# Optimization experiments

Measured on AMD Instinct MI355X. Metric: run time of the kernel, lower is better.

The kernel has to match this reference:

```python
import jax, jax.numpy as jnp
import numpy as np

B, S, T = 4, 512, 512
D, F, L, H, V = 512, 2048, 6, 8, 32000
HD = D // H


def setup_inputs() -> dict:
    key = jax.random.key(0)
    ks = list(jax.random.split(key, 16))
    it = iter(ks)

    def w(shape, scale=0.02):
        return jax.random.normal(next(it), shape, jnp.float32) * scale

    enc_in = jax.random.randint(next(it), (B, S), 0, V, dtype=jnp.int32)
    dec_in = jax.random.randint(next(it), (B, T), 0, V, dtype=jnp.int32)

    # sinusoidal positional encoding (make_sine_pos_encoding)
    pos = np.arange(S)[:, None].astype(np.float32)
    i = np.arange(D)[None, :].astype(np.float32)
    angle = pos / np.power(10000.0, (2.0 * np.floor(i / 2.0)) / D)
    pe = np.zeros((S, D), np.float32)
    pe[:, 0::2] = np.sin(angle[:, 0::2])
    pe[:, 1::2] = np.cos(angle[:, 1::2])

    return {
        "enc_in": enc_in,
        "dec_in": dec_in,
        "e_embed": w((V, D)),
        "d_embed": w((V, D)),
        "pos_enc": jnp.asarray(pe),
        "enc_mha_W": w((L, 4, D, D)),      # q,k,v,out
        "enc_mha_b": jnp.zeros((L, 4, D), jnp.float32),
        "enc_ln_g": jnp.ones((L, 2, D), jnp.float32),
        "enc_ln_b": jnp.zeros((L, 2, D), jnp.float32),
        "enc_ffn_W1": w((L, D, F)),
        "enc_ffn_b1": jnp.zeros((L, F), jnp.float32),
        "enc_ffn_W2": w((L, F, D)),
        "enc_ffn_b2": jnp.zeros((L, D), jnp.float32),
        "dec_mha_W": w((L, 8, D, D)),      # self q,k,v,out then cross q,k,v,out
        "dec_mha_b": jnp.zeros((L, 8, D), jnp.float32),
        "dec_ln_g": jnp.ones((L, 3, D), jnp.float32),
        "dec_ln_b": jnp.zeros((L, 3, D), jnp.float32),
        "dec_ffn_W1": w((L, D, F)),
        "dec_ffn_b1": jnp.zeros((L, F), jnp.float32),
        "dec_ffn_W2": w((L, F, D)),
        "dec_ffn_b2": jnp.zeros((L, D), jnp.float32),
    }


def _layer_norm(x, g, b, eps=1e-6):
    m = jnp.mean(x, axis=-1, keepdims=True)
    v = jnp.mean(jnp.square(x - m), axis=-1, keepdims=True)
    return (x - m) * jax.lax.rsqrt(v + eps) * g + b


def _split_heads(x):
    b, n, _ = x.shape
    return x.reshape(b, n, H, HD).transpose(0, 2, 1, 3)  # b h n d


def _mha(xq, xkv, W, b, mask):
    # W: [>=4, D, D] slice of (q,k,v,out); mask: broadcastable to [b,h,nq,nk]
    q = _split_heads(xq @ W[0] + b[0])
    k = _split_heads(xkv @ W[1] + b[1])
    v = _split_heads(xkv @ W[2] + b[2])
    s = jnp.einsum('bhqd,bhkd->bhqk', q, k) / jnp.sqrt(jnp.float32(HD))
    s = s + mask * (-1e9)
    a = jax.nn.softmax(s, axis=-1)
    o = jnp.einsum('bhqk,bhkd->bhqd', a, v)
    o = o.transpose(0, 2, 1, 3).reshape(xq.shape[0], xq.shape[1], D)
    return o @ W[3] + b[3]


def _forward(enc_in, dec_in, e_embed, d_embed, pos_enc,
             enc_mha_W, enc_mha_b, enc_ln_g, enc_ln_b,
             enc_ffn_W1, enc_ffn_b1, enc_ffn_W2, enc_ffn_b2,
             dec_mha_W, dec_mha_b, dec_ln_g, dec_ln_b,
             dec_ffn_W1, dec_ffn_b1, dec_ffn_W2, dec_ffn_b2):
    # masks: 1.0 where attention is blocked
    enc_pad = (enc_in == 0).astype(jnp.float32)[:, None, None, :]   # [B,1,1,S]
    dec_pad = (dec_in == 0).astype(jnp.float32)[:, None, None, :]   # [B,1,1,T]
    la = jnp.triu(jnp.ones((T, T), jnp.float32), k=1)[None, None]   # [1,1,T,T]
    look_ahead = jnp.maximum(la, dec_pad)                           # [B,1,T,T]

    scale = jnp.float32(D) ** 0.5
    e = e_embed[enc_in] * scale + pos_enc[None, :S]
    d = d_embed[dec_in] * scale + pos_enc[None, :T]

    for l in range(L):
        y = _mha(e, e, enc_mha_W[l], enc_mha_b[l], enc_pad)
        e = _layer_norm(e + y, enc_ln_g[l, 0], enc_ln_b[l, 0])
        y = jax.nn.relu(e @ enc_ffn_W1[l] + enc_ffn_b1[l]) @ enc_ffn_W2[l] + enc_ffn_b2[l]
        e = _layer_norm(e + y, enc_ln_g[l, 1], enc_ln_b[l, 1])

    for l in range(L):
        y = _mha(d, d, dec_mha_W[l, 0:4], dec_mha_b[l, 0:4], look_ahead)
        d = _layer_norm(d + y, dec_ln_g[l, 0], dec_ln_b[l, 0])
        y = _mha(d, e, dec_mha_W[l, 4:8], dec_mha_b[l, 4:8], enc_pad)
        d = _layer_norm(d + y, dec_ln_g[l, 1], dec_ln_b[l, 1])
        y = jax.nn.relu(d @ dec_ffn_W1[l] + dec_ffn_b1[l]) @ dec_ffn_W2[l] + dec_ffn_b2[l]
        d = _layer_norm(d + y, dec_ln_g[l, 2], dec_ln_b[l, 2])

    return d @ d_embed.T  # [B,T,V] logits


def reference(enc_in, dec_in, e_embed, d_embed, pos_enc,
              enc_mha_W, enc_mha_b, enc_ln_g, enc_ln_b,
              enc_ffn_W1, enc_ffn_b1, enc_ffn_W2, enc_ffn_b2,
              dec_mha_W, dec_mha_b, dec_ln_g, dec_ln_b,
              dec_ffn_W1, dec_ffn_b1, dec_ffn_W2, dec_ffn_b2):
    return _forward(enc_in, dec_in, e_embed, d_embed, pos_enc,
                    enc_mha_W, enc_mha_b, enc_ln_g, enc_ln_b,
                    enc_ffn_W1, enc_ffn_b1, enc_ffn_W2, enc_ffn_b2,
                    dec_mha_W, dec_mha_b, dec_ln_g, dec_ln_b,
                    dec_ffn_W1, dec_ffn_b1, dec_ffn_W2, dec_ffn_b2)
```

## Files before the change

### kernel.cpp

```cpp
#include <hip/hip_runtime.h>
#include <hip/hip_bf16.h>
#include <math.h>

#define B_ 4
#define S_ 512
#define D_ 512
#define F_ 2048
#define L_ 6
#define H_ 8
#define V_ 32000

typedef unsigned short u16;
typedef __attribute__((ext_vector_type(8))) short bhalf8;
typedef __attribute__((ext_vector_type(4))) float f32x4;

__device__ __forceinline__ u16 f2b(float v) {
    unsigned x = __builtin_bit_cast(unsigned, v);
    return (u16)((x + 0x7FFFu + ((x >> 16) & 1u)) >> 16);
}

#define GLD16(g, l) __builtin_amdgcn_global_load_lds( \
    (const __attribute__((address_space(1))) void*)(g), \
    (__attribute__((address_space(3))) void*)(l), 16, 0, 0)

__device__ __forceinline__ float redmax16(float v) {
    #pragma unroll
    for (int m = 1; m < 16; m <<= 1) v = fmaxf(v, __shfl_xor(v, m));
    return v;
}
__device__ __forceinline__ float redsum16(float v) {
    #pragma unroll
    for (int m = 1; m < 16; m <<= 1) v += __shfl_xor(v, m);
    return v;
}

template<int NWR, int NWC, int WM, int WN, int OUT, int RELU, int MLOOP, int SPLITA>
__global__ __launch_bounds__(NWR * NWC * 64)
void mfma_gemm(const u16* __restrict__ A, const u16* __restrict__ A2, int acut,
               const u16* __restrict__ B,
               const float* __restrict__ bias, void* __restrict__ Cv,
               int K, int lda, int ldb, int ldc,
               u16* __restrict__ vtp, int vc0)
{
    constexpr int BM = NWR * WM, BN = NWC * WN;
    constexpr int NW = NWR * NWC;
    constexpr int CH_A = BM / 16, CH_B = BN / 16, CH = CH_A + CH_B;
    constexpr int NI = WM / 16, NJ = WN / 16;

    __shared__ u16 As[BM * 32];
    __shared__ u16 Bs[BN * 32];

    const int tid = threadIdx.x;
    const int wid = tid >> 6, lane = tid & 63;
    const int wrow = wid / NWC, wcol = wid % NWC;
    const long bn = (long)blockIdx.x * BN;
    const int r4 = lane >> 2, c4 = lane & 3;
    const int l15 = lane & 15, l4 = lane >> 4;

    const u16* Ause = (SPLITA && bn >= acut) ? A2 : A;

    #pragma unroll 1
    for (int mi = 0; mi < MLOOP; ++mi) {
        const long bm = ((long)blockIdx.y * MLOOP + mi) * BM;

        f32x4 acc[NI][NJ];
        #pragma unroll
        for (int i = 0; i < NI; ++i)
            #pragma unroll
            for (int j = 0; j < NJ; ++j)
                acc[i][j] = (f32x4){0.f, 0.f, 0.f, 0.f};

        for (int k0 = 0; k0 < K; k0 += 32) {
            #pragma unroll
            for (int t = 0; t < CH / NW; ++t) {
                int c = wid + t * NW;
                if (c < CH_A) {
                    const u16* g = Ause + (bm + c * 16 + r4) * (long)lda + k0 + c4 * 8;
                    GLD16(g, As + c * 512 + lane * 8);
                } else {
                    int cb = c - CH_A;
                    const u16* g = B + (bn + cb * 16 + r4) * (long)ldb + k0 + c4 * 8;
                    GLD16(g, Bs + cb * 512 + lane * 8);
                }
            }
            __syncthreads();
            bhalf8 af[NI], bfr[NJ];
            #pragma unroll
            for (int i = 0; i < NI; ++i)
                af[i] = *(const bhalf8*)&As[(wrow * WM + i * 16 + l15) * 32 + l4 * 8];
            #pragma unroll
            for (int j = 0; j < NJ; ++j)
                bfr[j] = *(const bhalf8*)&Bs[(wcol * WN + j * 16 + l15) * 32 + l4 * 8];
            #pragma unroll
            for (int i = 0; i < NI; ++i)
                #pragma unroll
                for (int j = 0; j < NJ; ++j)
                    acc[i][j] = __builtin_amdgcn_mfma_f32_16x16x32_bf16(af[i], bfr[j], acc[i][j], 0, 0, 0);
            __syncthreads();
        }

        float* Cf = (float*)Cv;
        u16*   Cb = (u16*)Cv;
        const int rowb = wrow * WM + (l4 << 2);
        const int colb = wcol * WN + l15;
        #pragma unroll
        for (int j = 0; j < NJ; ++j) {
            const long gcb = bn + wcol * WN + j * 16;
            const bool tovt = (vtp != nullptr) && (gcb >= vc0);
            const long gc = bn + colb + j * 16;
            const float bv = bias ? bias[gc] : 0.f;
            #pragma unroll
            for (int i = 0; i < NI; ++i) {
                const long gr = bm + rowb + i * 16;
                #pragma unroll
                for (int r = 0; r < 4; ++r) {
                    float v = acc[i][j][r] + bv;
                    if (RELU) v = fmaxf(v, 0.f);
                    if (tovt)          vtp[(gc - vc0) * 2048 + gr + r] = f2b(v);
                    else if (OUT == 0) Cf[(gr + r) * (long)ldc + gc] = v;
                    else               Cb[(gr + r) * (long)ldc + gc] = f2b(v);
                }
            }
        }
    }
}

template<int CAUSAL>
__global__ __launch_bounds__(256)
void flash_kernel(const u16* __restrict__ Qp, int ldq,
                  const u16* __restrict__ Kp, int ldk,
                  const u16* __restrict__ Vt,
                  const int* __restrict__ tok,
                  u16* __restrict__ Op)
{
    __shared__ u16 QS[64 * 64];
    __shared__ u16 KS[64 * 64];
    __shared__ u16 VS[64 * 64];
    __shared__ u16 PS[4 * 16 * 64];
    __shared__ float MK[512];

    const int tid = threadIdx.x, lane = tid & 63, w = tid >> 6;
    const int l15 = lane & 15, l4 = lane >> 4;
    const int qb = blockIdx.x, bh = blockIdx.y;
    const int b = bh >> 3, h = bh & 7;

    const u16* Q = Qp + (long)(b * 512 + qb * 64) * ldq + h * 64;
    const u16* K = Kp + (long)(b * 512) * ldk + h * 64;
    const u16* V = Vt + (long)(h * 64) * 2048 + b * 512;
    u16* O = Op + (long)(b * 512 + qb * 64) * 512 + h * 64;

    {
        int t0 = tok[b * 512 + tid];
        int t1 = tok[b * 512 + 256 + tid];
        MK[tid]       = (t0 == 0) ? -1e9f : 0.f;
        MK[tid + 256] = (t1 == 0) ? -1e9f : 0.f;
    }
    {
        int r = tid >> 3;
        int c = (tid & 7) ^ (r & 7);
        GLD16(Q + (long)r * ldq + c * 8,        QS + tid * 8);
        GLD16(Q + (long)(r + 32) * ldq + c * 8, QS + 2048 + tid * 8);
    }

    f32x4 oacc[4];
    float mrun[4], lrun[4];
    #pragma unroll
    for (int j = 0; j < 4; ++j) oacc[j] = (f32x4){0.f, 0.f, 0.f, 0.f};
    #pragma unroll
    for (int r = 0; r < 4; ++r) { mrun[r] = -1e30f; lrun[r] = 0.f; }

    bhalf8 qa[2];
    const int tmax = CAUSAL ? qb : 7;

    for (int t = 0; t <= tmax; ++t) {
        {
            int r = tid >> 3;
            int c = (tid & 7) ^ (r & 7);
            GLD16(K + (long)(t * 64 + r) * ldk + c * 8,       KS + tid * 8);
            GLD16(K + (long)(t * 64 + 32 + r) * ldk + c * 8,  KS + 2048 + tid * 8);
            GLD16(V + (long)r * 2048 + t * 64 + c * 8,        VS + tid * 8);
            GLD16(V + (long)(r + 32) * 2048 + t * 64 + c * 8, VS + 2048 + tid * 8);
        }
        __syncthreads();
        if (t == 0) {
            #pragma unroll
            for (int kc = 0; kc < 2; ++kc) {
                int row = w * 16 + l15;
                qa[kc] = *(const bhalf8*)&QS[row * 64 + (((kc * 4 + l4) ^ (row & 7)) << 3)];
            }
        }
        f32x4 sac[4];
        #pragma unroll
        for (int jj = 0; jj < 4; ++jj) sac[jj] = (f32x4){0.f, 0.f, 0.f, 0.f};
        bhalf8 kf[4][2];
        #pragma unroll
        for (int jj = 0; jj < 4; ++jj)
            #pragma unroll
            for (int kc = 0; kc < 2; ++kc) {
                int row = jj * 16 + l15;
                kf[jj][kc] = *(const bhalf8*)&KS[row * 64 + (((kc * 4 + l4) ^ (row & 7)) << 3)];
            }
        #pragma unroll
        for (int jj = 0; jj < 4; ++jj)
            #pragma unroll
            for (int kc = 0; kc < 2; ++kc)
                sac[jj] = __builtin_amdgcn_mfma_f32_16x16x32_bf16(qa[kc], kf[jj][kc], sac[jj], 0, 0, 0);

        #pragma unroll
        for (int jj = 0; jj < 4; ++jj) {
            float mk = MK[t * 64 + jj * 16 + l15];
            #pragma unroll
            for (int r = 0; r < 4; ++r) {
                float mk2 = mk;
                if (CAUSAL && t == qb) {
                    int col = t * 64 + jj * 16 + l15;
                    int qr = qb * 64 + w * 16 + l4 * 4 + r;
                    if (col > qr) mk2 = -1e9f;
                }
                sac[jj][r] = sac[jj][r] * 0.125f + mk2;
            }
        }
        #pragma unroll
        for (int r = 0; r < 4; ++r) {
            float mx = fmaxf(fmaxf(sac[0][r], sac[1][r]), fmaxf(sac[2][r], sac[3][r]));
            mx = redmax16(mx);
            float mnew = fmaxf(mrun[r], mx);
            float alpha = __expf(mrun[r] - mnew);
            float sum = 0.f;
            int row_p = l4 * 4 + r;
            #pragma unroll
            for (int jj = 0; jj < 4; ++jj) {
                float pv = __expf(sac[jj][r] - mnew);
                sum += pv;
                int kv = jj * 16 + l15;
                PS[w * 1024 + row_p * 64 + ((((kv >> 3) ^ (row_p & 7)) << 3) | (kv & 7))] = f2b(pv);
            }
            sum = redsum16(sum);
            lrun[r] = lrun[r] * alpha + sum;
            mrun[r] = mnew;
            #pragma unroll
            for (int jd = 0; jd < 4; ++jd) oacc[jd][r] *= alpha;
        }
        bhalf8 pa[2], vf[4][2];
        #pragma unroll
        for (int kc = 0; kc < 2; ++kc) {
            int row = l15;
            pa[kc] = *(const bhalf8*)&PS[w * 1024 + row * 64 + (((kc * 4 + l4) ^ (row & 7)) << 3)];
        }
        #pragma unroll
        for (int jd = 0; jd < 4; ++jd)
            #pragma unroll
            for (int kc = 0; kc < 2; ++kc) {
                int row = jd * 16 + l15;
                vf[jd][kc] = *(const bhalf8*)&VS[row * 64 + (((kc * 4 + l4) ^ (row & 7)) << 3)];
            }
        #pragma unroll
        for (int jd = 0; jd < 4; ++jd)
            #pragma unroll
            for (int kc = 0; kc < 2; ++kc)
                oacc[jd] = __builtin_amdgcn_mfma_f32_16x16x32_bf16(pa[kc], vf[jd][kc], oacc[jd], 0, 0, 0);
        __syncthreads();
    }

    #pragma unroll
    for (int r = 0; r < 4; ++r) {
        float inv = 1.f / lrun[r];
        int row = w * 16 + l4 * 4 + r;
        #pragma unroll
        for (int jd = 0; jd < 4; ++jd)
            O[(long)row * 512 + jd * 16 + l15] = f2b(oacc[jd][r] * inv);
    }
}

__global__ __launch_bounds__(256)
void transpose_many(const float* __restrict__ inA, const float* __restrict__ inB,
                    int zsplit, int R, int C, u16* __restrict__ out)
{
    int z = blockIdx.z;
    const float* in = (z < zsplit) ? inA + (long)z * R * C
                                   : inB + (long)(z - zsplit) * R * C;
    u16* o = out + (long)z * R * C;
    __shared__ float tb[64][65];
    const int tr = blockIdx.y * 64, tc = blockIdx.x * 64;
    const int col = threadIdx.x & 63, r0 = threadIdx.x >> 6;
    #pragma unroll
    for (int p = 0; p < 16; ++p) {
        int row = r0 * 16 + p;
        tb[row][col] = in[(long)(tr + row) * C + tc + col];
    }
    __syncthreads();
    #pragma unroll
    for (int p = 0; p < 16; ++p) {
        int row = r0 * 16 + p;
        o[(long)(tc + row) * R + tr + col] = f2b(tb[col][row]);
    }
}

__global__ __launch_bounds__(256)
void convert_b16(const float4* __restrict__ in, u16* __restrict__ out, long n4)
{
    long i = (long)blockIdx.x * 256 + threadIdx.x;
    if (i >= n4) return;
    float4 v = in[i];
    uint2 p;
    p.x = (unsigned)f2b(v.x) | ((unsigned)f2b(v.y) << 16);
    p.y = (unsigned)f2b(v.z) | ((unsigned)f2b(v.w) << 16);
    *(uint2*)(out + i * 4) = p;
}

__global__ __launch_bounds__(256)
void embed_kernel(const int* __restrict__ tE, const int* __restrict__ tD,
                  const float* __restrict__ eE, const float* __restrict__ eD,
                  const float* __restrict__ pos,
                  float* __restrict__ xE, float* __restrict__ xD,
                  u16* __restrict__ bE, u16* __restrict__ bD, float scale)
{
    const int z = blockIdx.y;
    const int* tok = z ? tD : tE;
    const float* emb = z ? eD : eE;
    float* x = z ? xD : xE;
    u16* xb = z ? bD : bE;
    int row = blockIdx.x;
    int s = row & (S_ - 1);
    int t = tok[row];
    const float* er = emb + (long)t * D_;
    const float* pr = pos + (long)s * D_;
    float* o = x + (long)row * D_;
    u16*  ob = xb + (long)row * D_;
    int i = threadIdx.x;
    float v0 = er[i]       * scale + pr[i];
    float v1 = er[i + 256] * scale + pr[i + 256];
    o[i] = v0;        o[i + 256] = v1;
    ob[i] = f2b(v0);  ob[i + 256] = f2b(v1);
}

__global__ __launch_bounds__(256)
void add_ln_kernel(float* __restrict__ x, const float* __restrict__ y,
                   u16* __restrict__ xb,
                   const float* __restrict__ g, const float* __restrict__ bb)
{
    long row = blockIdx.x;
    float* xr = x + row * D_;
    u16* xo = xb + row * D_;
    const float* yr = y + row * D_;
    int t = threadIdx.x, t2 = t + 256;

    float r0 = xr[t] + yr[t];
    float r1 = xr[t2] + yr[t2];
    float s = r0 + r1;
    float s2 = r0 * r0 + r1 * r1;
    #pragma unroll
    for (int i = 1; i < 64; i <<= 1) {
        s  += __shfl_xor(s, i);
        s2 += __shfl_xor(s2, i);
    }
    __shared__ float rs[4], rs2[4];
    int wid = t >> 6;
    if ((t & 63) == 0) { rs[wid] = s; rs2[wid] = s2; }
    __syncthreads();
    s  = rs[0] + rs[1] + rs[2] + rs[3];
    s2 = rs2[0] + rs2[1] + rs2[2] + rs2[3];

    float mean = s * (1.f / D_);
    float var  = s2 * (1.f / D_) - mean * mean;
    float inv  = rsqrtf(var + 1e-6f);
    float o0 = (r0 - mean) * inv * g[t]  + bb[t];
    float o1 = (r1 - mean) * inv * g[t2] + bb[t2];
    xr[t] = o0;       xr[t2] = o1;
    xo[t] = f2b(o0);  xo[t2] = f2b(o1);
}

extern "C" void kernel_launch(void* const* d_in, const int* in_sizes, int n_in,
                              void* d_out, int out_size, void* d_ws, size_t ws_size,
                              hipStream_t stream)
{
    const int*   enc_in     = (const int*)  d_in[0];
    const int*   dec_in     = (const int*)  d_in[1];
    const float* e_embed    = (const float*)d_in[2];
    const float* d_embed    = (const float*)d_in[3];
    const float* pos_enc    = (const float*)d_in[4];
    const float* enc_mha_W  = (const float*)d_in[5];
    const float* enc_mha_b  = (const float*)d_in[6];
    const float* enc_ln_g   = (const float*)d_in[7];
    const float* enc_ln_b   = (const float*)d_in[8];
    const float* enc_ffn_W1 = (const float*)d_in[9];
    const float* enc_ffn_b1 = (const float*)d_in[10];
    const float* enc_ffn_W2 = (const float*)d_in[11];
    const float* enc_ffn_b2 = (const float*)d_in[12];
    const float* dec_mha_W  = (const float*)d_in[13];
    const float* dec_mha_b  = (const float*)d_in[14];
    const float* dec_ln_g   = (const float*)d_in[15];
    const float* dec_ln_b   = (const float*)d_in[16];
    const float* dec_ffn_W1 = (const float*)d_in[17];
    const float* dec_ffn_b1 = (const float*)d_in[18];
    const float* dec_ffn_W2 = (const float*)d_in[19];
    const float* dec_ffn_b2 = (const float*)d_in[20];
    float* out = (float*)d_out;

    const int  BS  = B_ * S_;
    const long BSD = (long)BS * D_;
    const long DD  = (long)D_ * D_;
    const long DF  = (long)D_ * F_;

    char* p = (char*)d_ws;
    auto alloc = [&](long bytes) { char* r = p; p += (bytes + 255) & ~255L; return r; };
    float* e    = (float*)alloc(BSD * 4);
    float* dd   = (float*)alloc(BSD * 4);
    float* y    = (float*)alloc(BSD * 4);
    u16*   eb   = (u16*)  alloc(BSD * 2);
    u16*   ddb  = (u16*)  alloc(BSD * 2);
    u16*   qkv  = (u16*)  alloc((long)BS * 1536 * 2);
    u16*   att  = (u16*)  alloc(BSD * 2);
    u16*   vt   = (u16*)  alloc(BSD * 2);
    u16*   ffnh = (u16*)  alloc((long)BS * F_ * 2);
    u16*   wEmb = (u16*)  alloc((long)V_ * D_ * 2);
    u16*   wMha = (u16*)  alloc(72 * DD * 2);
    u16*   wF1  = (u16*)  alloc(12 * DF * 2);
    u16*   wF2  = (u16*)  alloc(12 * DF * 2);

    transpose_many<<<dim3(8, 8, 72), 256, 0, stream>>>(enc_mha_W, dec_mha_W, 24, 512, 512, wMha);
    transpose_many<<<dim3(32, 8, 12), 256, 0, stream>>>(enc_ffn_W1, dec_ffn_W1, 6, 512, 2048, wF1);
    transpose_many<<<dim3(8, 32, 12), 256, 0, stream>>>(enc_ffn_W2, dec_ffn_W2, 6, 2048, 512, wF2);
    convert_b16<<<16000, 256, 0, stream>>>((const float4*)d_embed, wEmb, (long)V_ * D_ / 4);

    const float scale = sqrtf((float)D_);
    embed_kernel<<<dim3(BS, 2), 256, 0, stream>>>(enc_in, dec_in, e_embed, d_embed,
                                                  pos_enc, e, dd, eb, ddb, scale);

    #define GEMM_BIG(grid, RELU, OUTT, A, Bp, bias, C, K, lda, ldb, ldc) \
        mfma_gemm<2,2,64,64,OUTT,RELU,1,0><<<grid, 256, 0, stream>>>(A, A, 1 << 30, Bp, bias, C, K, lda, ldb, ldc, nullptr, 0)
    #define GEMM_SK(grid, OUTT, A, Bp, bias, C, K, lda, ldb, ldc, vtp, vc0) \
        mfma_gemm<2,1,32,64,OUTT,0,1,0><<<grid, 128, 0, stream>>>(A, A, 1 << 30, Bp, bias, C, K, lda, ldb, ldc, vtp, vc0)

    for (int l = 0; l < L_; ++l) {
        const u16* Wl = wMha + (long)l * 4 * DD;
        const float* bl = enc_mha_b + (long)l * 4 * D_;
        GEMM_SK(dim3(24, 32), 1, eb, Wl, bl, qkv, 512, 512, 512, 1536, vt, 1024);
        flash_kernel<0><<<dim3(8, 32), 256, 0, stream>>>(qkv, 1536, qkv + 512, 1536, vt, enc_in, att);
        GEMM_SK(dim3(8, 32), 0, att, Wl + 3 * DD, bl + 3 * D_, y, 512, 512, 512, 512, nullptr, 0);
        add_ln_kernel<<<BS, 256, 0, stream>>>(e, y, eb,
            enc_ln_g + (long)(l * 2) * D_, enc_ln_b + (long)(l * 2) * D_);
        GEMM_BIG(dim3(16, 16), 1, 1, eb, wF1 + (long)l * DF, enc_ffn_b1 + (long)l * F_,
                 ffnh, 512, 512, 512, 2048);
        GEMM_SK(dim3(8, 32), 0, ffnh, wF2 + (long)l * DF, enc_ffn_b2 + (long)l * D_,
                y, 2048, 2048, 2048, 512, nullptr, 0);
        add_ln_kernel<<<BS, 256, 0, stream>>>(e, y, eb,
            enc_ln_g + (long)(l * 2 + 1) * D_, enc_ln_b + (long)(l * 2 + 1) * D_);
    }

    for (int l = 0; l < L_; ++l) {
        const u16* Wl = wMha + (long)(24 + l * 8) * DD;
        const float* bl = dec_mha_b + (long)l * 8 * D_;
        GEMM_SK(dim3(24, 32), 1, ddb, Wl, bl, qkv, 512, 512, 512, 1536, vt, 1024);
        flash_kernel<1><<<dim3(8, 32), 256, 0, stream>>>(qkv, 1536, qkv + 512, 1536, vt, dec_in, att);
        GEMM_SK(dim3(8, 32), 0, att, Wl + 3 * DD, bl + 3 * D_, y, 512, 512, 512, 512, nullptr, 0);
        add_ln_kernel<<<BS, 256, 0, stream>>>(dd, y, ddb,
            dec_ln_g + (long)(l * 3) * D_, dec_ln_b + (long)(l * 3) * D_);
        mfma_gemm<2,1,32,64,1,0,1,1><<<dim3(24, 32), 128, 0, stream>>>(
            ddb, eb, 512, Wl + 4 * DD, bl + 4 * D_, qkv,
            512, 512, 512, 1536, vt, 1024);
        flash_kernel<0><<<dim3(8, 32), 256, 0, stream>>>(qkv, 1536, qkv + 512, 1536, vt, enc_in, att);
        GEMM_SK(dim3(8, 32), 0, att, Wl + 7 * DD, bl + 7 * D_, y, 512, 512, 512, 512, nullptr, 0);
        add_ln_kernel<<<BS, 256, 0, stream>>>(dd, y, ddb,
            dec_ln_g + (long)(l * 3 + 1) * D_, dec_ln_b + (long)(l * 3 + 1) * D_);
        GEMM_BIG(dim3(16, 16), 1, 1, ddb, wF1 + (long)(6 + l) * DF, dec_ffn_b1 + (long)l * F_,
                 ffnh, 512, 512, 512, 2048);
        GEMM_SK(dim3(8, 32), 0, ffnh, wF2 + (long)(6 + l) * DF, dec_ffn_b2 + (long)l * D_,
                y, 2048, 2048, 2048, 512, nullptr, 0);
        add_ln_kernel<<<BS, 256, 0, stream>>>(dd, y, ddb,
            dec_ln_g + (long)(l * 3 + 2) * D_, dec_ln_b + (long)(l * 3 + 2) * D_);
    }

    mfma_gemm<2,2,64,64,0,0,8,0><<<dim3(250, 2), 256, 0, stream>>>(
        ddb, ddb, 1 << 30, wEmb, nullptr, out, 512, 512, 512, 32000, nullptr, 0);
}
```

Before: 1.864 ms.

## Fuse attention out-projection with residual LayerNorm and stage V-transpose through LDS

Adds a gemm_ln_kernel in which one block computes 16 full rows of the attention output projection and then applies bias, residual add and LayerNorm in place. This removes the separate y round-trip and the add_ln launch after each attention block. The V-transpose epilogue now goes through an LDS tile so vt gets coalesced 16-byte stores. The final vocab GEMM switches to an x-major grid without the M loop and uses nontemporal stores. The fused kernel runs only 128 blocks and computes variance as E[x^2]-mean^2, which can lose some precision.

```diff
diff --git a/kernel.cpp b/kernel.cpp
--- a/kernel.cpp
+++ b/kernel.cpp
@@ -34,7 +34,8 @@
     return v;
 }
 
-template<int NWR, int NWC, int WM, int WN, int OUT, int RELU, int MLOOP, int SPLITA>
+template<int NWR, int NWC, int WM, int WN, int OUT, int RELU, int MLOOP,
+         int SPLITA, int XMAJOR, int NT, int VTT>
 __global__ __launch_bounds__(NWR * NWC * 64)
 void mfma_gemm(const u16* __restrict__ A, const u16* __restrict__ A2, int acut,
                const u16* __restrict__ B,
@@ -49,11 +50,13 @@
 
     __shared__ u16 As[BM * 32];
     __shared__ u16 Bs[BN * 32];
+    __shared__ u16 TT[VTT ? 64 * 72 : 8];
 
     const int tid = threadIdx.x;
     const int wid = tid >> 6, lane = tid & 63;
     const int wrow = wid / NWC, wcol = wid % NWC;
-    const long bn = (long)blockIdx.x * BN;
+    const long bn = (XMAJOR ? (long)blockIdx.y : (long)blockIdx.x) * BN;
+    const long bmbase = (XMAJOR ? (long)blockIdx.x : (long)blockIdx.y);
     const int r4 = lane >> 2, c4 = lane & 3;
     const int l15 = lane & 15, l4 = lane >> 4;
 
@@ -61,7 +64,7 @@
 
     #pragma unroll 1
     for (int mi = 0; mi < MLOOP; ++mi) {
-        const long bm = ((long)blockIdx.y * MLOOP + mi) * BM;
+        const long bm = (bmbase * MLOOP + mi) * BM;
 
         f32x4 acc[NI][NJ];
         #pragma unroll
@@ -99,14 +102,38 @@
             __syncthreads();
         }
 
+        if (VTT && vtp != nullptr && bn >= vc0) {
+            #pragma unroll
+            for (int j = 0; j < NJ; ++j) {
+                const int c = wcol * WN + j * 16 + l15;
+                const float bv = bias ? bias[bn + c] : 0.f;
+                #pragma unroll
+                for (int i = 0; i < NI; ++i) {
+                    const int rw = wrow * WM + i * 16 + (l4 << 2);
+                    #pragma unroll
+                    for (int r = 0; r < 4; ++r)
+                        TT[c * 72 + rw + r] = f2b(acc[i][j][r] + bv);
+                }
+            }
+            __syncthreads();
+            {
+                const int c = tid >> 1, hh = tid & 1;
+                const u16* src = &TT[c * 72 + hh * 32];
+                u16* dst = &vtp[(bn - vc0 + c) * 2048 + bm + hh * 32];
+                #pragma unroll
+                for (int p = 0; p < 4; ++p)
+                    *(uint4*)(dst + p * 8) = *(const uint4*)(src + p * 8);
+            }
+            __syncthreads();
+            continue;
+        }
+
         float* Cf = (float*)Cv;
         u16*   Cb = (u16*)Cv;
         const int rowb = wrow * WM + (l4 << 2);
         const int colb = wcol * WN + l15;
         #pragma unroll
         for (int j = 0; j < NJ; ++j) {
-            const long gcb = bn + wcol * WN + j * 16;
-            const bool tovt = (vtp != nullptr) && (gcb >= vc0);
             const long gc = bn + colb + j * 16;
             const float bv = bias ? bias[gc] : 0.f;
             #pragma unroll
@@ -116,11 +143,105 @@
                 for (int r = 0; r < 4; ++r) {
                     float v = acc[i][j][r] + bv;
                     if (RELU) v = fmaxf(v, 0.f);
-                    if (tovt)          vtp[(gc - vc0) * 2048 + gr + r] = f2b(v);
-                    else if (OUT == 0) Cf[(gr + r) * (long)ldc + gc] = v;
-                    else               Cb[(gr + r) * (long)ldc + gc] = f2b(v);
+                    if (OUT == 0) {
+                        if (NT) __builtin_nontemporal_store(v, &Cf[(gr + r) * (long)ldc + gc]);
+                        else    Cf[(gr + r) * (long)ldc + gc] = v;
+                    } else {
+                        Cb[(gr + r) * (long)ldc + gc] = f2b(v);
+                    }
                 }
             }
+        }
+    }
+}
+
+__global__ __launch_bounds__(512)
+void gemm_ln_kernel(const u16* __restrict__ A, const u16* __restrict__ B,
+                    const float* __restrict__ bias,
+                    float* __restrict__ x, u16* __restrict__ xb,
+                    const float* __restrict__ g, const float* __restrict__ bb,
+                    int K)
+{
+    __shared__ u16 As[16 * 32];
+    __shared__ u16 Bs[512 * 32];
+    __shared__ float red[2][16][8];
+    __shared__ float mv[2][16];
+
+    const int tid = threadIdx.x, w = tid >> 6, lane = tid & 63;
+    const int l15 = lane & 15, l4 = lane >> 4;
+    const int r4 = lane >> 2, c4 = lane & 3;
+    const long bm = (long)blockIdx.x * 16;
+
+    f32x4 acc[4];
+    #pragma unroll
+    for (int j = 0; j < 4; ++j) acc[j] = (f32x4){0.f, 0.f, 0.f, 0.f};
+
+    for (int k0 = 0; k0 < K; k0 += 32) {
+        #pragma unroll
+        for (int t = 0; t < 5; ++t) {
+            int c = w + t * 8;
+            if (c < 33) {
+                if (c == 0) {
+                    GLD16(A + (bm + r4) * (long)K + k0 + c4 * 8, As + lane * 8);
+                } else {
+                    GLD16(B + ((c - 1) * 16 + r4) * (long)K + k0 + c4 * 8,
+                          Bs + (c - 1) * 512 + lane * 8);
+                }
+            }
+        }
+        __syncthreads();
+        bhalf8 af = *(const bhalf8*)&As[l15 * 32 + l4 * 8];
+        #pragma unroll
+        for (int j = 0; j < 4; ++j) {
+            bhalf8 bf = *(const bhalf8*)&Bs[(w * 64 + j * 16 + l15) * 32 + l4 * 8];
+            acc[j] = __builtin_amdgcn_mfma_f32_16x16x32_bf16(af, bf, acc[j], 0, 0, 0);
+        }
+        __syncthreads();
+    }
+
+    float vbuf[4][4], s[4] = {0, 0, 0, 0}, s2[4] = {0, 0, 0, 0};
+    #pragma unroll
+    for (int j = 0; j < 4; ++j) {
+        int col = w * 64 + j * 16 + l15;
+        float bv = bias[col];
+        #pragma unroll
+        for (int r = 0; r < 4; ++r) {
+            int row = l4 * 4 + r;
+            float v = acc[j][r] + bv + x[(bm + row) * 512 + col];
+            vbuf[j][r] = v;
+            s[r] += v; s2[r] += v * v;
+        }
+    }
+    #pragma unroll
+    for (int r = 0; r < 4; ++r) { s[r] = redsum16(s[r]); s2[r] = redsum16(s2[r]); }
+    if (l15 == 0) {
+        #pragma unroll
+        for (int r = 0; r < 4; ++r) {
+            red[0][l4 * 4 + r][w] = s[r];
+            red[1][l4 * 4 + r][w] = s2[r];
+        }
+    }
+    __syncthreads();
+    if (tid < 16) {
+        float S = 0.f, S2 = 0.f;
+        #pragma unroll
+        for (int q = 0; q < 8; ++q) { S += red[0][tid][q]; S2 += red[1][tid][q]; }
+        float mean = S * (1.f / 512.f);
+        float var = S2 * (1.f / 512.f) - mean * mean;
+        mv[0][tid] = mean;
+        mv[1][tid] = rsqrtf(var + 1e-6f);
+    }
+    __syncthreads();
+    #pragma unroll
+    for (int j = 0; j < 4; ++j) {
+        int col = w * 64 + j * 16 + l15;
+        float gg = g[col], bbv = bb[col];
+        #pragma unroll
+        for (int r = 0; r < 4; ++r) {
+            int row = l4 * 4 + r;
+            float o = (vbuf[j][r] - mv[0][row]) * mv[1][row] * gg + bbv;
+            x[(bm + row) * 512 + col] = o;
+            xb[(bm + row) * 512 + col] = f2b(o);
         }
     }
 }
@@ -428,22 +549,23 @@
                                                   pos_enc, e, dd, eb, ddb, scale);
 
     #define GEMM_BIG(grid, RELU, OUTT, A, Bp, bias, C, K, lda, ldb, ldc) \
-        mfma_gemm<2,2,64,64,OUTT,RELU,1,0><<<grid, 256, 0, stream>>>(A, A, 1 << 30, Bp, bias, C, K, lda, ldb, ldc, nullptr, 0)
-    #define GEMM_SK(grid, OUTT, A, Bp, bias, C, K, lda, ldb, ldc, vtp, vc0) \
-        mfma_gemm<2,1,32,64,OUTT,0,1,0><<<grid, 128, 0, stream>>>(A, A, 1 << 30, Bp, bias, C, K, lda, ldb, ldc, vtp, vc0)
+        mfma_gemm<2,2,64,64,OUTT,RELU,1,0,0,0,0><<<grid, 256, 0, stream>>>(A, A, 1 << 30, Bp, bias, C, K, lda, ldb, ldc, nullptr, 0)
+    #define GEMM_SKV(grid, A, Bp, bias, C, K, lda, ldb, ldc, vtp, vc0) \
+        mfma_gemm<2,1,32,64,1,0,1,0,0,0,1><<<grid, 128, 0, stream>>>(A, A, 1 << 30, Bp, bias, C, K, lda, ldb, ldc, vtp, vc0)
+    #define GEMM_SK(grid, OUTT, A, Bp, bias, C, K, lda, ldb, ldc) \
+        mfma_gemm<2,1,32,64,OUTT,0,1,0,0,0,0><<<grid, 128, 0, stream>>>(A, A, 1 << 30, Bp, bias, C, K, lda, ldb, ldc, nullptr, 0)
 
     for (int l = 0; l < L_; ++l) {
         const u16* Wl = wMha + (long)l * 4 * DD;
         const float* bl = enc_mha_b + (long)l * 4 * D_;
-        GEMM_SK(dim3(24, 32), 1, eb, Wl, bl, qkv, 512, 512, 512, 1536, vt, 1024);
+        GEMM_SKV(dim3(24, 32), eb, Wl, bl, qkv, 512, 512, 512, 1536, vt, 1024);
         flash_kernel<0><<<dim3(8, 32), 256, 0, stream>>>(qkv, 1536, qkv + 512, 1536, vt, enc_in, att);
-        GEMM_SK(dim3(8, 32), 0, att, Wl + 3 * DD, bl + 3 * D_, y, 512, 512, 512, 512, nullptr, 0);
-        add_ln_kernel<<<BS, 256, 0, stream>>>(e, y, eb,
-            enc_ln_g + (long)(l * 2) * D_, enc_ln_b + (long)(l * 2) * D_);
+        gemm_ln_kernel<<<128, 512, 0, stream>>>(att, Wl + 3 * DD, bl + 3 * D_,
+            e, eb, enc_ln_g + (long)(l * 2) * D_, enc_ln_b + (long)(l * 2) * D_, 512);
         GEMM_BIG(dim3(16, 16), 1, 1, eb, wF1 + (long)l * DF, enc_ffn_b1 + (long)l * F_,
                  ffnh, 512, 512, 512, 2048);
         GEMM_SK(dim3(8, 32), 0, ffnh, wF2 + (long)l * DF, enc_ffn_b2 + (long)l * D_,
-                y, 2048, 2048, 2048, 512, nullptr, 0);
+                y, 2048, 2048, 2048, 512);
         add_ln_kernel<<<BS, 256, 0, stream>>>(e, y, eb,
             enc_ln_g + (long)(l * 2 + 1) * D_, enc_ln_b + (long)(l * 2 + 1) * D_);
     }
@@ -451,26 +573,24 @@
     for (int l = 0; l < L_; ++l) {
         const u16* Wl = wMha + (long)(24 + l * 8) * DD;
         const float* bl = dec_mha_b + (long)l * 8 * D_;
-        GEMM_SK(dim3(24, 32), 1, ddb, Wl, bl, qkv, 512, 512, 512, 1536, vt, 1024);
+        GEMM_SKV(dim3(24, 32), ddb, Wl, bl, qkv, 512, 512, 512, 1536, vt, 1024);
         flash_kernel<1><<<dim3(8, 32), 256, 0, stream>>>(qkv, 1536, qkv + 512, 1536, vt, dec_in, att);
-        GEMM_SK(dim3(8, 32), 0, att, Wl + 3 * DD, bl + 3 * D_, y, 512, 512, 512, 512, nullptr, 0);
-        add_ln_kernel<<<BS, 256, 0, stream>>>(dd, y, ddb,
-            dec_ln_g + (long)(l * 3) * D_, dec_ln_b + (long)(l * 3) * D_);
-        mfma_gemm<2,1,32,64,1,0,1,1><<<dim3(24, 32), 128, 0, stream>>>(
+        gemm_ln_kernel<<<128, 512, 0, stream>>>(att, Wl + 3 * DD, bl + 3 * D_,
+            dd, ddb, dec_ln_g + (long)(l * 3) * D_, dec_ln_b + (long)(l * 3) * D_, 512);
+        mfma_gemm<2,1,32,64,1,0,1,1,0,0,1><<<dim3(24, 32), 128, 0, stream>>>(
             ddb, eb, 512, Wl + 4 * DD, bl + 4 * D_, qkv,
             512, 512, 512, 1536, vt, 1024);
         flash_kernel<0><<<dim3(8, 32), 256, 0, stream>>>(qkv, 1536, qkv + 512, 1536, vt, enc_in, att);
-        GEMM_SK(dim3(8, 32), 0, att, Wl + 7 * DD, bl + 7 * D_, y, 512, 512, 512, 512, nullptr, 0);
-        add_ln_kernel<<<BS, 256, 0, stream>>>(dd, y, ddb,
-            dec_ln_g + (long)(l * 3 + 1) * D_, dec_ln_b + (long)(l * 3 + 1) * D_);
+        gemm_ln_kernel<<<128, 512, 0, stream>>>(att, Wl + 7 * DD, bl + 7 * D_,
+            dd, ddb, dec_ln_g + (long)(l * 3 + 1) * D_, dec_ln_b + (long)(l * 3 + 1) * D_, 512);
         GEMM_BIG(dim3(16, 16), 1, 1, ddb, wF1 + (long)(6 + l) * DF, dec_ffn_b1 + (long)l * F_,
                  ffnh, 512, 512, 512, 2048);
         GEMM_SK(dim3(8, 32), 0, ffnh, wF2 + (long)(6 + l) * DF, dec_ffn_b2 + (long)l * D_,
-                y, 2048, 2048, 2048, 512, nullptr, 0);
+                y, 2048, 2048, 2048, 512);
         add_ln_kernel<<<BS, 256, 0, stream>>>(dd, y, ddb,
             dec_ln_g + (long)(l * 3 + 2) * D_, dec_ln_b + (long)(l * 3 + 2) * D_);
     }
 
-    mfma_gemm<2,2,64,64,0,0,8,0><<<dim3(250, 2), 256, 0, stream>>>(
+    mfma_gemm<2,2,64,64,0,0,1,0,1,1,0><<<dim3(16, 250), 256, 0, stream>>>(
         ddb, ddb, 1 << 30, wEmb, nullptr, out, 512, 512, 512, 32000, nullptr, 0);
 }
```

After: 1.805 ms. -3.1%, faster.
